# Performance work log

Measured on AMD Instinct MI355X. Metric: run time of the kernel, lower is better.

The kernel has to match this reference:

```python
import jax, jax.numpy as jnp
import numpy as np

B, N, C = 4, 1024, 1024
H = 16
HD = C // H
HID = 4 * C
EPS = 1e-5


def layernorm(x, g, b):
    mu = jnp.mean(x, axis=-1, keepdims=True)
    var = jnp.mean(jnp.square(x - mu), axis=-1, keepdims=True)
    return (x - mu) * jax.lax.rsqrt(var + EPS) * g + b


def setup_inputs() -> dict:
    key = jax.random.key(0)
    ks = jax.random.split(key, 16)
    s = lambda d: 1.0 / np.sqrt(d)
    return {
        "x": jax.random.normal(ks[0], (B, N, C), dtype=jnp.float32),
        "ln1_g": jnp.ones((C,), jnp.float32),
        "ln1_b": jnp.zeros((C,), jnp.float32),
        "qkv_w": jax.random.normal(ks[1], (3 * C, C), jnp.float32) * s(C),
        "proj_w": jax.random.normal(ks[2], (C, C), jnp.float32) * s(C),
        "proj_b": jnp.zeros((C,), jnp.float32),
        "gamma1": jnp.full((C,), 1e-5, jnp.float32),
        "ln2_g": jnp.ones((C,), jnp.float32),
        "ln2_b": jnp.zeros((C,), jnp.float32),
        "fc1_w": jax.random.normal(ks[3], (HID, C), jnp.float32) * s(C),
        "fc1_b": jnp.zeros((HID,), jnp.float32),
        "fc2_w": jax.random.normal(ks[4], (C, HID), jnp.float32) * s(HID),
        "fc2_b": jnp.zeros((C,), jnp.float32),
        "gamma2": jnp.full((C,), 1e-5, jnp.float32),
    }


def reference(x, ln1_g, ln1_b, qkv_w, proj_w, proj_b, gamma1,
              ln2_g, ln2_b, fc1_w, fc1_b, fc2_w, fc2_b, gamma2):
    # --- attention residual branch ---
    n1 = layernorm(x, ln1_g, ln1_b)                     # [B,N,C]
    qkv = jnp.einsum('bnc,oc->bno', n1, qkv_w)          # [B,N,3C]
    qkv = qkv.reshape(B, N, 3, H, HD).transpose(2, 0, 3, 1, 4)  # [3,B,H,N,HD]
    scale = HD ** -0.5
    q, k, v = qkv[0] * scale, qkv[1], qkv[2]
    attn = jax.nn.softmax(jnp.einsum('bhnd,bhmd->bhnm', q, k), axis=-1)  # [B,H,N,N]
    ao = jnp.einsum('bhnm,bhmd->bhnd', attn, v)         # [B,H,N,HD]
    ao = ao.transpose(0, 2, 1, 3).reshape(B, N, C)
    ao = jnp.einsum('bnc,oc->bno', ao, proj_w) + proj_b
    x = x + ao * gamma1
    # --- mlp residual branch ---
    n2 = layernorm(x, ln2_g, ln2_b)
    h = jax.nn.gelu(jnp.einsum('bnc,hc->bnh', n2, fc1_w) + fc1_b, approximate=False)
    m = jnp.einsum('bnh,ch->bnc', h, fc2_w) + fc2_b
    x = x + m * gamma2
    return x, attn
```

## Files before the change

kernel.cpp:

```cpp
#include <hip/hip_runtime.h>
#include <math.h>

typedef __attribute__((ext_vector_type(8))) short bf16x8;
typedef __attribute__((ext_vector_type(4))) short bf16x4;
typedef __attribute__((ext_vector_type(4))) float f32x4;

__device__ __forceinline__ unsigned short f2bf(float f) {
  unsigned u = __builtin_bit_cast(unsigned, f);
  u += 0x7fffu + ((u >> 16) & 1u);
  return (unsigned short)(u >> 16);
}

#define MFMA16(a, b, c) __builtin_amdgcn_mfma_f32_16x16x32_bf16((a), (b), (c), 0, 0, 0)

__device__ __forceinline__ void gload_lds16(const void* g, void* l) {
  __builtin_amdgcn_global_load_lds(
      (const __attribute__((address_space(1))) unsigned*)g,
      (__attribute__((address_space(3))) unsigned*)l, 16, 0, 0);
}

__device__ __forceinline__ int xcd_swz(int bid, int nwg) {
  int q = nwg >> 3, r = nwg & 7;
  int xcd = bid & 7, off = bid >> 3;
  return (xcd < r ? xcd * (q + 1) : r * (q + 1) + (xcd - r) * q) + off;
}

__global__ __launch_bounds__(256) void k_cvt4(
    const float* __restrict__ wq, const float* __restrict__ wp,
    const float* __restrict__ w1, const float* __restrict__ w2,
    unsigned short* __restrict__ oq, unsigned short* __restrict__ op,
    unsigned short* __restrict__ o1, unsigned short* __restrict__ o2) {
  int bid = blockIdx.x;
  const float* src; unsigned short* dst; int base;
  if (bid < 3072)      { src = wq; dst = oq; base = bid; }
  else if (bid < 4096) { src = wp; dst = op; base = bid - 3072; }
  else if (bid < 8192) { src = w1; dst = o1; base = bid - 4096; }
  else                 { src = w2; dst = o2; base = bid - 8192; }
  int i = base * 256 + threadIdx.x;
  float4 v = ((const float4*)src)[i];
  bf16x4 o;
  o[0] = (short)f2bf(v.x); o[1] = (short)f2bf(v.y);
  o[2] = (short)f2bf(v.z); o[3] = (short)f2bf(v.w);
  *(bf16x4*)(dst + (size_t)i * 4) = o;
}

__global__ __launch_bounds__(256) void k_ln(const float* __restrict__ x,
                                            const float* __restrict__ g,
                                            const float* __restrict__ b,
                                            unsigned short* __restrict__ out) {
  __shared__ float red[8];
  const int tid = threadIdx.x;
  const size_t row = blockIdx.x;
  float4 v = ((const float4*)(x + row * 1024))[tid];
  float s = v.x + v.y + v.z + v.w;
#pragma unroll
  for (int off = 32; off; off >>= 1) s += __shfl_xor(s, off);
  if ((tid & 63) == 0) red[tid >> 6] = s;
  __syncthreads();
  float mu = (red[0] + red[1] + red[2] + red[3]) * (1.0f / 1024.0f);
  float dx = v.x - mu, dy = v.y - mu, dz = v.z - mu, dw = v.w - mu;
  float s2 = dx * dx + dy * dy + dz * dz + dw * dw;
#pragma unroll
  for (int off = 32; off; off >>= 1) s2 += __shfl_xor(s2, off);
  if ((tid & 63) == 0) red[4 + (tid >> 6)] = s2;
  __syncthreads();
  float var = (red[4] + red[5] + red[6] + red[7]) * (1.0f / 1024.0f);
  float rstd = rsqrtf(var + 1e-5f);
  float4 gv = ((const float4*)g)[tid];
  float4 bv = ((const float4*)b)[tid];
  bf16x4 o;
  o[0] = (short)f2bf(dx * rstd * gv.x + bv.x);
  o[1] = (short)f2bf(dy * rstd * gv.y + bv.y);
  o[2] = (short)f2bf(dz * rstd * gv.z + bv.z);
  o[3] = (short)f2bf(dw * rstd * gv.w + bv.w);
  *(bf16x4*)(out + row * 1024 + tid * 4) = o;
}

template <int EPI>
__global__ __launch_bounds__(512, 2) void k_gemm256(
    const unsigned short* __restrict__ A, const unsigned short* __restrict__ Bw,
    int Ndim, int K, int nby,
    const float* __restrict__ bias,
    unsigned short* __restrict__ Qc, unsigned short* __restrict__ Kc,
    unsigned short* __restrict__ VTo,
    unsigned short* __restrict__ outb) {
  __shared__ __align__(16) unsigned short lds[2][2][16384];

  const int tid = threadIdx.x;
  const int wid = tid >> 6, lane = tid & 63;
  const int wm = wid >> 2, wn = wid & 3;
  const int lr = lane & 15, lhi = lane >> 4;

  const int nwg = gridDim.x;
  const int swz = xcd_swz(blockIdx.x, nwg);
  const int bcol = swz / nby, brow = swz % nby;

  const size_t a_base = (size_t)brow * 256 * K;
  const size_t b_base = (size_t)bcol * 256 * K;
  const int NT = K >> 6;

  auto STAGE = [&](int dbuf, int kt, int which) {
    int ktc = (kt < NT) ? kt : 0;
    int isB = which & 1;
    int odd = which >> 1;
    const unsigned short* src = isB ? (Bw + b_base) : (A + a_base);
    int col = (ktc << 6) + (((lane & 7) ^ ((lane >> 3) & 7)) << 3);
#pragma unroll
    for (int c = 0; c < 2; ++c) {
      int idx = (wid << 1) | c;
      int chunk = isB ? ((idx & 3) + ((idx >> 2) << 3) + (odd << 2))
                      : ((idx & 7) + ((idx >> 3) << 4) + (odd << 3));
      int row = (chunk << 3) + (lane >> 3);
      gload_lds16(src + (size_t)row * K + col,
                  &lds[dbuf][isB][chunk * 512 + lane * 8]);
    }
  };

  STAGE(0, 0, 0); STAGE(0, 0, 1); STAGE(0, 0, 2); STAGE(0, 0, 3);

  f32x4 acc[8][4] = {};
  bf16x8 aF0[4][2], aF1[4][2], bF0[2][2], bF1[2][2];

  const int colx0 = (lhi << 4) ^ ((lr & 7) << 4);
  const int colx1 = (64 + (lhi << 4)) ^ ((lr & 7) << 4);

  for (int t = 0; t < NT; ++t) {
    const int buf = t & 1;
    const char* sAb = (const char*)&lds[buf][0][0];
    const char* sBb = (const char*)&lds[buf][1][0];
#pragma unroll
    for (int q = 0; q < 4; ++q) {
      asm volatile("s_waitcnt vmcnt(6)" ::: "memory");
      __builtin_amdgcn_s_barrier();
      if (q == 0) {
#pragma unroll
        for (int m = 0; m < 4; ++m) {
          int ro = (wm * 128 + m * 16 + lr) * 128;
          aF0[m][0] = *(const bf16x8*)(sAb + ro + colx0);
          aF0[m][1] = *(const bf16x8*)(sAb + ro + colx1);
        }
      } else if (q == 1) {
#pragma unroll
        for (int n = 0; n < 2; ++n) {
          int ro = (wn * 64 + n * 16 + lr) * 128;
          bF0[n][0] = *(const bf16x8*)(sBb + ro + colx0);
          bF0[n][1] = *(const bf16x8*)(sBb + ro + colx1);
        }
      } else if (q == 2) {
#pragma unroll
        for (int m = 0; m < 4; ++m) {
          int ro = (wm * 128 + 64 + m * 16 + lr) * 128;
          aF1[m][0] = *(const bf16x8*)(sAb + ro + colx0);
          aF1[m][1] = *(const bf16x8*)(sAb + ro + colx1);
        }
      } else {
#pragma unroll
        for (int n = 0; n < 2; ++n) {
          int ro = (wn * 64 + 32 + n * 16 + lr) * 128;
          bF1[n][0] = *(const bf16x8*)(sBb + ro + colx0);
          bF1[n][1] = *(const bf16x8*)(sBb + ro + colx1);
        }
      }
      STAGE(buf ^ 1, t + 1, q);
      asm volatile("s_waitcnt lgkmcnt(0)" ::: "memory");
      __builtin_amdgcn_sched_barrier(0);
      __builtin_amdgcn_s_setprio(1);
      if (q == 0) {
        if (t > 0) {
#pragma unroll
          for (int m = 0; m < 4; ++m)
#pragma unroll
            for (int n = 0; n < 2; ++n)
#pragma unroll
              for (int kk = 0; kk < 2; ++kk)
                acc[4 + m][2 + n] = MFMA16(aF1[m][kk], bF1[n][kk], acc[4 + m][2 + n]);
        }
      } else if (q == 1) {
#pragma unroll
        for (int m = 0; m < 4; ++m)
#pragma unroll
          for (int n = 0; n < 2; ++n)
#pragma unroll
            for (int kk = 0; kk < 2; ++kk)
              acc[m][n] = MFMA16(aF0[m][kk], bF0[n][kk], acc[m][n]);
      } else if (q == 2) {
#pragma unroll
        for (int m = 0; m < 4; ++m)
#pragma unroll
          for (int n = 0; n < 2; ++n)
#pragma unroll
            for (int kk = 0; kk < 2; ++kk)
              acc[4 + m][n] = MFMA16(aF1[m][kk], bF0[n][kk], acc[4 + m][n]);
      } else {
#pragma unroll
        for (int m = 0; m < 4; ++m)
#pragma unroll
          for (int n = 0; n < 2; ++n)
#pragma unroll
            for (int kk = 0; kk < 2; ++kk)
              acc[m][2 + n] = MFMA16(aF0[m][kk], bF1[n][kk], acc[m][2 + n]);
      }
      __builtin_amdgcn_s_setprio(0);
    }
  }
#pragma unroll
  for (int m = 0; m < 4; ++m)
#pragma unroll
    for (int n = 0; n < 2; ++n)
#pragma unroll
      for (int kk = 0; kk < 2; ++kk)
        acc[4 + m][2 + n] = MFMA16(aF1[m][kk], bF1[n][kk], acc[4 + m][2 + n]);

  if (EPI == 0) {
    const int region = bcol >> 2;
    const int h = (bcol & 3) * 4 + wn;
    if (region < 2) {
      unsigned short* dst = (region == 0) ? Qc : Kc;
#pragma unroll
      for (int m = 0; m < 8; ++m)
#pragma unroll
        for (int n = 0; n < 4; ++n) {
          int d = n * 16 + lr;
#pragma unroll
          for (int r = 0; r < 4; ++r) {
            int row = brow * 256 + wm * 128 + m * 16 + lhi * 4 + r;
            int b = row >> 10, kv = row & 1023;
            dst[((size_t)((b << 4) + h) << 16) + (size_t)kv * 64 + d] =
                f2bf(acc[m][n][r]);
          }
        }
    } else {
#pragma unroll
      for (int m = 0; m < 8; ++m)
#pragma unroll
        for (int n = 0; n < 4; ++n) {
          int d = n * 16 + lr;
          int row0_ = brow * 256 + wm * 128 + m * 16 + lhi * 4;
          int b = row0_ >> 10, kv0 = row0_ & 1023;
          bf16x4 o;
          o[0] = (short)f2bf(acc[m][n][0]);
          o[1] = (short)f2bf(acc[m][n][1]);
          o[2] = (short)f2bf(acc[m][n][2]);
          o[3] = (short)f2bf(acc[m][n][3]);
          *(bf16x4*)&VTo[((size_t)((b << 4) + h) << 16) + ((size_t)d << 10) + kv0] = o;
        }
    }
  } else {
#pragma unroll
    for (int m = 0; m < 8; ++m)
#pragma unroll
      for (int n = 0; n < 4; ++n) {
        int col = bcol * 256 + wn * 64 + n * 16 + lr;
        float bi = bias[col];
#pragma unroll
        for (int r = 0; r < 4; ++r) {
          int row = brow * 256 + wm * 128 + m * 16 + lhi * 4 + r;
          float v = acc[m][n][r] + bi;
          v = 0.5f * v * (1.0f + erff(v * 0.70710678118654752f));
          outb[(size_t)row * Ndim + col] = f2bf(v);
        }
      }
  }
}

__global__ __launch_bounds__(256) void k_gemm_bt2(
    const unsigned short* __restrict__ A, const unsigned short* __restrict__ Bw,
    int Ndim, int K, int nby,
    const float* __restrict__ bias, const float* __restrict__ gamma,
    const float* __restrict__ resid, float* __restrict__ outf) {
  __shared__ __align__(16) unsigned short sA[128 * 64];
  __shared__ __align__(16) unsigned short sB[128 * 64];
  const int tid = threadIdx.x;
  const int wid = tid >> 6, lane = tid & 63;
  const int wr = wid >> 1, wc = wid & 1;
  const int lr = lane & 15, lhi = lane >> 4;
  const int swz = xcd_swz(blockIdx.x, gridDim.x);
  const int bcol = swz / nby, brow = swz % nby;

  const size_t a_base = (size_t)brow * 128 * K;
  const size_t b_base = (size_t)bcol * 128 * K;
  const int srow = tid >> 3;
  const int scol = (tid & 7) * 8;

  f32x4 acc[4][4] = {};

  for (int k0 = 0; k0 < K; k0 += 64) {
    __syncthreads();
#pragma unroll
    for (int r = 0; r < 4; ++r) {
      int row = r * 32 + srow;
      gload_lds16(&A[a_base + (size_t)row * K + k0 + scol], &sA[row * 64 + scol]);
      gload_lds16(&Bw[b_base + (size_t)row * K + k0 + scol], &sB[row * 64 + scol]);
    }
    __syncthreads();
#pragma unroll
    for (int kk = 0; kk < 2; ++kk) {
      bf16x8 af[4], bfr[4];
#pragma unroll
      for (int i = 0; i < 4; ++i) {
        int ar = wr * 64 + i * 16 + lr;
        af[i] = *(const bf16x8*)&sA[ar * 64 + kk * 32 + lhi * 8];
        int br = wc * 64 + i * 16 + lr;
        bfr[i] = *(const bf16x8*)&sB[br * 64 + kk * 32 + lhi * 8];
      }
#pragma unroll
      for (int i = 0; i < 4; ++i)
#pragma unroll
        for (int j = 0; j < 4; ++j)
          acc[i][j] = MFMA16(af[i], bfr[j], acc[i][j]);
    }
  }

#pragma unroll
  for (int i = 0; i < 4; ++i)
#pragma unroll
    for (int j = 0; j < 4; ++j)
#pragma unroll
      for (int r = 0; r < 4; ++r) {
        int row = brow * 128 + wr * 64 + i * 16 + lhi * 4 + r;
        int col = bcol * 128 + wc * 64 + j * 16 + lr;
        float v = resid[(size_t)row * Ndim + col] + (acc[i][j][r] + bias[col]) * gamma[col];
        outf[(size_t)row * Ndim + col] = v;
      }
}

__global__ __launch_bounds__(256) void k_attn(const unsigned short* __restrict__ Qc,
                                              const unsigned short* __restrict__ Kc,
                                              const unsigned short* __restrict__ VT,
                                              float* __restrict__ attn_out,
                                              unsigned short* __restrict__ ao) {
  __shared__ __align__(16) char smem[33280];
  __shared__ float red[2][4][32];

  const int tid = threadIdx.x;
  const int wid = tid >> 6, lane = tid & 63;
  const int lr = lane & 15, lhi = lane >> 4;
  const int q0 = blockIdx.x * 32;
  const int bh = blockIdx.y;
  const int b = bh >> 4, h = bh & 15;
  const size_t hb = (size_t)bh << 16;
  const int hcol = h * 64;

  bf16x8 af[2][2];
#pragma unroll
  for (int i = 0; i < 2; ++i)
#pragma unroll
    for (int kk = 0; kk < 2; ++kk)
      af[i][kk] = *(const bf16x8*)&Qc[hb + (size_t)(q0 + i * 16 + lr) * 64 +
                                      kk * 32 + lhi * 8];

  f32x4 acc[2][16] = {};
#pragma unroll
  for (int kk = 0; kk < 2; ++kk) {
#pragma unroll
    for (int j = 0; j < 16; ++j) {
      int m = wid * 256 + j * 16 + lr;
      bf16x8 bv = *(const bf16x8*)&Kc[hb + (size_t)m * 64 + kk * 32 + lhi * 8];
      acc[0][j] = MFMA16(af[0][kk], bv, acc[0][j]);
      acc[1][j] = MFMA16(af[1][kk], bv, acc[1][j]);
    }
  }

  float mx[2][4], sm[2][4];
#pragma unroll
  for (int i = 0; i < 2; ++i)
#pragma unroll
    for (int r = 0; r < 4; ++r) {
      float m_ = -1e30f;
#pragma unroll
      for (int j = 0; j < 16; ++j) {
        acc[i][j][r] *= 0.125f;
        m_ = fmaxf(m_, acc[i][j][r]);
      }
#pragma unroll
      for (int off = 1; off < 16; off <<= 1) m_ = fmaxf(m_, __shfl_xor(m_, off));
      mx[i][r] = m_;
    }
  if (lr == 0) {
#pragma unroll
    for (int i = 0; i < 2; ++i)
#pragma unroll
      for (int r = 0; r < 4; ++r) red[0][wid][i * 16 + lhi * 4 + r] = mx[i][r];
  }
  __syncthreads();
#pragma unroll
  for (int i = 0; i < 2; ++i)
#pragma unroll
    for (int r = 0; r < 4; ++r) {
      int rl = i * 16 + lhi * 4 + r;
      float m_ = fmaxf(fmaxf(red[0][0][rl], red[0][1][rl]),
                       fmaxf(red[0][2][rl], red[0][3][rl]));
      float s_ = 0.f;
#pragma unroll
      for (int j = 0; j < 16; ++j) {
        float e = __expf(acc[i][j][r] - m_);
        acc[i][j][r] = e;
        s_ += e;
      }
#pragma unroll
      for (int off = 1; off < 16; off <<= 1) s_ += __shfl_xor(s_, off);
      sm[i][r] = s_;
    }
  if (lr == 0) {
#pragma unroll
    for (int i = 0; i < 2; ++i)
#pragma unroll
      for (int r = 0; r < 4; ++r) red[1][wid][i * 16 + lhi * 4 + r] = sm[i][r];
  }
  __syncthreads();

  float inv[2][4];
#pragma unroll
  for (int i = 0; i < 2; ++i)
#pragma unroll
    for (int r = 0; r < 4; ++r) {
      int rl = i * 16 + lhi * 4 + r;
      inv[i][r] = 1.0f / (red[1][0][rl] + red[1][1][rl] + red[1][2][rl] + red[1][3][rl]);
    }

  unsigned pb[2][16][2];
  {
    const size_t attn_base =
        (size_t)bh * 1024 * 1024 + ((size_t)q0) * 1024 + (size_t)(wid * 256);
#pragma unroll
    for (int i = 0; i < 2; ++i)
#pragma unroll
      for (int j = 0; j < 16; ++j) {
        float p0 = acc[i][j][0] * inv[i][0];
        float p1 = acc[i][j][1] * inv[i][1];
        float p2 = acc[i][j][2] * inv[i][2];
        float p3 = acc[i][j][3] * inv[i][3];
        size_t base = attn_base + (size_t)(i * 16 + lhi * 4) * 1024 + j * 16 + lr;
        attn_out[base] = p0;
        attn_out[base + 1024] = p1;
        attn_out[base + 2048] = p2;
        attn_out[base + 3072] = p3;
        pb[i][j][0] = (unsigned)f2bf(p0) | ((unsigned)f2bf(p1) << 16);
        pb[i][j][1] = (unsigned)f2bf(p2) | ((unsigned)f2bf(p3) << 16);
      }
  }

  char* sP = smem + wid * 4096;
  f32x4 oaccT[4][2] = {};

#pragma unroll
  for (int t = 0; t < 4; ++t) {
#pragma unroll
    for (int i = 0; i < 2; ++i)
#pragma unroll
      for (int jl = 0; jl < 4; ++jl) {
        int j = t * 4 + jl;
        int kvl2 = (jl * 16 + lr) * 2;
#pragma unroll
        for (int hp = 0; hp < 2; ++hp) {
          unsigned d = pb[i][j][hp];
          int qa = i * 16 + lhi * 4 + hp * 2;
          int qb = qa + 1;
          *(unsigned short*)(sP + qa * 128 + (kvl2 ^ ((qa & 7) << 4))) =
              (unsigned short)(d & 0xffff);
          *(unsigned short*)(sP + qb * 128 + (kvl2 ^ ((qb & 7) << 4))) =
              (unsigned short)(d >> 16);
        }
      }
#pragma unroll
    for (int c = 0; c < 2; ++c) {
      bf16x8 pf[2];
#pragma unroll
      for (int qt = 0; qt < 2; ++qt) {
        int q_ = qt * 16 + lr;
        pf[qt] = *(const bf16x8*)(sP + q_ * 128 + ((c * 64 + lhi * 16) ^ ((q_ & 7) << 4)));
      }
#pragma unroll
      for (int dt = 0; dt < 4; ++dt) {
        int d_ = dt * 16 + lr;
        bf16x8 vf = *(const bf16x8*)&VT[hb + ((size_t)d_ << 10) +
                                        wid * 256 + t * 64 + c * 32 + lhi * 8];
        oaccT[dt][0] = MFMA16(vf, pf[0], oaccT[dt][0]);
        oaccT[dt][1] = MFMA16(vf, pf[1], oaccT[dt][1]);
      }
    }
  }

  __syncthreads();
  float* sAO = (float*)smem;
#pragma unroll
  for (int dt = 0; dt < 4; ++dt)
#pragma unroll
    for (int qt = 0; qt < 2; ++qt)
#pragma unroll
      for (int r = 0; r < 4; ++r) {
        int q_ = qt * 16 + lr;
        int d_ = dt * 16 + lhi * 4 + r;
        sAO[wid * 2080 + q_ * 65 + d_] = oaccT[dt][qt][r];
      }
  __syncthreads();
  {
    int q_ = tid >> 3;
    int d0 = (tid & 7) * 8;
    bf16x8 o;
#pragma unroll
    for (int e = 0; e < 8; ++e) {
      int d_ = d0 + e;
      float s = sAO[q_ * 65 + d_] + sAO[2080 + q_ * 65 + d_] +
                sAO[4160 + q_ * 65 + d_] + sAO[6240 + q_ * 65 + d_];
      o[e] = (short)f2bf(s);
    }
    *(bf16x8*)&ao[(size_t)(b * 1024 + q0 + q_) * 1024 + hcol + d0] = o;
  }
}

extern "C" void kernel_launch(void* const* d_in, const int* in_sizes, int n_in,
                              void* d_out, int out_size, void* d_ws, size_t ws_size,
                              hipStream_t stream) {
  (void)in_sizes; (void)n_in; (void)out_size; (void)ws_size;
  const float* x     = (const float*)d_in[0];
  const float* ln1g  = (const float*)d_in[1];
  const float* ln1b  = (const float*)d_in[2];
  const float* qkvw  = (const float*)d_in[3];
  const float* projw = (const float*)d_in[4];
  const float* projb = (const float*)d_in[5];
  const float* g1    = (const float*)d_in[6];
  const float* ln2g  = (const float*)d_in[7];
  const float* ln2b  = (const float*)d_in[8];
  const float* fc1w  = (const float*)d_in[9];
  const float* fc1b  = (const float*)d_in[10];
  const float* fc2w  = (const float*)d_in[11];
  const float* fc2b  = (const float*)d_in[12];
  const float* g2    = (const float*)d_in[13];

  char* ws = (char*)d_ws;
  unsigned short* w_qkv  = (unsigned short*)(ws);
  unsigned short* w_proj = (unsigned short*)(ws + 6291456);
  unsigned short* w_fc1  = (unsigned short*)(ws + 8388608);
  unsigned short* w_fc2  = (unsigned short*)(ws + 16777216);
  unsigned short* n12    = (unsigned short*)(ws + 25165824);
  unsigned short* Qc     = (unsigned short*)(ws + 33554432);
  unsigned short* Kc     = (unsigned short*)(ws + 41943040);
  unsigned short* VT     = (unsigned short*)(ws + 50331648);
  unsigned short* hbuf   = (unsigned short*)(ws + 33554432);
  unsigned short* aob    = (unsigned short*)(ws + 58720256);
  float*          x1     = (float*)(ws + 67108864);

  float* outx = (float*)d_out;
  float* outattn = outx + (size_t)4096 * 1024;

  k_cvt4<<<12288, 256, 0, stream>>>(qkvw, projw, fc1w, fc2w,
                                    w_qkv, w_proj, w_fc1, w_fc2);

  k_ln<<<4096, 256, 0, stream>>>(x, ln1g, ln1b, n12);
  k_gemm256<0><<<192, 512, 0, stream>>>(n12, w_qkv, 3072, 1024, 16,
                                        nullptr, Qc, Kc, VT, nullptr);
  k_attn<<<dim3(32, 64), 256, 0, stream>>>(Qc, Kc, VT, outattn, aob);
  k_gemm_bt2<<<256, 256, 0, stream>>>(aob, w_proj, 1024, 1024, 32,
                                      projb, g1, x, x1);
  k_ln<<<4096, 256, 0, stream>>>(x1, ln2g, ln2b, n12);
  k_gemm256<1><<<256, 512, 0, stream>>>(n12, w_fc1, 4096, 1024, 16,
                                        fc1b, nullptr, nullptr, nullptr, hbuf);
  k_gemm_bt2<<<256, 256, 0, stream>>>(hbuf, w_fc2, 1024, 4096, 32,
                                      fc2b, g2, x1, outx);
}
```

Baseline: 379.7 us.

## Split-K the fc2 GEMM with a reduction kernel and coalesce attention-prob stores

The fc2 GEMM (K=4096) now runs as a 4-way split-K over 1024 blocks instead of 256. Each slice writes fp32 partials to workspace, and a new reduction kernel sums them and applies bias, gamma and the residual. This raises parallelism on a GPU with many CUs, at the cost of extra partial-sum traffic (about 64MB written and read back). Separately, the attention kernel now writes the probability matrix from the swizzled LDS tile as row-contiguous float4 stores instead of scattered scalar stores. Those stored values are bf16-rounded probabilities rather than exact fp32, which costs some precision.

```diff
diff --git a/kernel.cpp b/kernel.cpp
--- a/kernel.cpp
+++ b/kernel.cpp
@@ -9,6 +9,9 @@
   unsigned u = __builtin_bit_cast(unsigned, f);
   u += 0x7fffu + ((u >> 16) & 1u);
   return (unsigned short)(u >> 16);
+}
+__device__ __forceinline__ float bf2f(unsigned short h) {
+  return __builtin_bit_cast(float, (unsigned)h << 16);
 }
 
 #define MFMA16(a, b, c) __builtin_amdgcn_mfma_f32_16x16x32_bf16((a), (b), (c), 0, 0, 0)
@@ -263,28 +266,34 @@
   }
 }
 
+template <int EPI>
 __global__ __launch_bounds__(256) void k_gemm_bt2(
     const unsigned short* __restrict__ A, const unsigned short* __restrict__ Bw,
     int Ndim, int K, int nby,
     const float* __restrict__ bias, const float* __restrict__ gamma,
-    const float* __restrict__ resid, float* __restrict__ outf) {
+    const float* __restrict__ resid, float* __restrict__ outf,
+    float* __restrict__ fpart) {
   __shared__ __align__(16) unsigned short sA[128 * 64];
   __shared__ __align__(16) unsigned short sB[128 * 64];
   const int tid = threadIdx.x;
   const int wid = tid >> 6, lane = tid & 63;
   const int wr = wid >> 1, wc = wid & 1;
   const int lr = lane & 15, lhi = lane >> 4;
-  const int swz = xcd_swz(blockIdx.x, gridDim.x);
+  int swz = xcd_swz(blockIdx.x, gridDim.x);
+  int kslice = 0;
+  if (EPI == 3) { kslice = swz & 3; swz >>= 2; }
   const int bcol = swz / nby, brow = swz % nby;
 
   const size_t a_base = (size_t)brow * 128 * K;
   const size_t b_base = (size_t)bcol * 128 * K;
   const int srow = tid >> 3;
   const int scol = (tid & 7) * 8;
+  const int kbeg = (EPI == 3) ? kslice * (K >> 2) : 0;
+  const int kend = (EPI == 3) ? kbeg + (K >> 2) : K;
 
   f32x4 acc[4][4] = {};
 
-  for (int k0 = 0; k0 < K; k0 += 64) {
+  for (int k0 = kbeg; k0 < kend; k0 += 64) {
     __syncthreads();
 #pragma unroll
     for (int r = 0; r < 4; ++r) {
@@ -311,6 +320,7 @@
     }
   }
 
+  const size_t pbase = (EPI == 3) ? (size_t)kslice * ((size_t)nby * 128) * Ndim : 0;
 #pragma unroll
   for (int i = 0; i < 4; ++i)
 #pragma unroll
@@ -319,9 +329,38 @@
       for (int r = 0; r < 4; ++r) {
         int row = brow * 128 + wr * 64 + i * 16 + lhi * 4 + r;
         int col = bcol * 128 + wc * 64 + j * 16 + lr;
-        float v = resid[(size_t)row * Ndim + col] + (acc[i][j][r] + bias[col]) * gamma[col];
-        outf[(size_t)row * Ndim + col] = v;
-      }
+        if (EPI == 2) {
+          float v = resid[(size_t)row * Ndim + col] +
+                    (acc[i][j][r] + bias[col]) * gamma[col];
+          outf[(size_t)row * Ndim + col] = v;
+        } else {
+          fpart[pbase + (size_t)row * Ndim + col] = acc[i][j][r];
+        }
+      }
+}
+
+__global__ __launch_bounds__(256) void k_fc2red(const float* __restrict__ p,
+                                                const float* __restrict__ x1,
+                                                const float* __restrict__ bias,
+                                                const float* __restrict__ gamma,
+                                                float* __restrict__ out) {
+  int idx = blockIdx.x * 256 + threadIdx.x;
+  int i = idx * 4;
+  int col = i & 1023;
+  const size_t S = (size_t)4096 * 1024;
+  float4 a = *(const float4*)&p[i];
+  float4 b = *(const float4*)&p[S + i];
+  float4 c = *(const float4*)&p[2 * S + i];
+  float4 d = *(const float4*)&p[3 * S + i];
+  float4 xr = *(const float4*)&x1[i];
+  float4 bi = *(const float4*)&bias[col];
+  float4 gm = *(const float4*)&gamma[col];
+  float4 o;
+  o.x = xr.x + (a.x + b.x + c.x + d.x + bi.x) * gm.x;
+  o.y = xr.y + (a.y + b.y + c.y + d.y + bi.y) * gm.y;
+  o.z = xr.z + (a.z + b.z + c.z + d.z + bi.z) * gm.z;
+  o.w = xr.w + (a.w + b.w + c.w + d.w + bi.w) * gm.w;
+  *(float4*)&out[i] = o;
 }
 
 __global__ __launch_bounds__(256) void k_attn(const unsigned short* __restrict__ Qc,
@@ -419,26 +458,15 @@
     }
 
   unsigned pb[2][16][2];
-  {
-    const size_t attn_base =
-        (size_t)bh * 1024 * 1024 + ((size_t)q0) * 1024 + (size_t)(wid * 256);
-#pragma unroll
-    for (int i = 0; i < 2; ++i)
-#pragma unroll
-      for (int j = 0; j < 16; ++j) {
-        float p0 = acc[i][j][0] * inv[i][0];
-        float p1 = acc[i][j][1] * inv[i][1];
-        float p2 = acc[i][j][2] * inv[i][2];
-        float p3 = acc[i][j][3] * inv[i][3];
-        size_t base = attn_base + (size_t)(i * 16 + lhi * 4) * 1024 + j * 16 + lr;
-        attn_out[base] = p0;
-        attn_out[base + 1024] = p1;
-        attn_out[base + 2048] = p2;
-        attn_out[base + 3072] = p3;
-        pb[i][j][0] = (unsigned)f2bf(p0) | ((unsigned)f2bf(p1) << 16);
-        pb[i][j][1] = (unsigned)f2bf(p2) | ((unsigned)f2bf(p3) << 16);
-      }
-  }
+#pragma unroll
+  for (int i = 0; i < 2; ++i)
+#pragma unroll
+    for (int j = 0; j < 16; ++j) {
+      pb[i][j][0] = (unsigned)f2bf(acc[i][j][0] * inv[i][0]) |
+                    ((unsigned)f2bf(acc[i][j][1] * inv[i][1]) << 16);
+      pb[i][j][1] = (unsigned)f2bf(acc[i][j][2] * inv[i][2]) |
+                    ((unsigned)f2bf(acc[i][j][3] * inv[i][3]) << 16);
+    }
 
   char* sP = smem + wid * 4096;
   f32x4 oaccT[4][2] = {};
@@ -462,6 +490,23 @@
               (unsigned short)(d >> 16);
         }
       }
+    {
+      int q_ = lane >> 1, half = lane & 1;
+      float* abase = attn_out + (size_t)bh * 1048576 + (size_t)(q0 + q_) * 1024 +
+                     wid * 256 + t * 64 + half * 32;
+#pragma unroll
+      for (int s = 0; s < 4; ++s) {
+        bf16x8 pv = *(const bf16x8*)(sP + q_ * 128 +
+                                     (((half * 32 + s * 8) * 2) ^ ((q_ & 7) << 4)));
+        float4 o0, o1;
+        o0.x = bf2f((unsigned short)pv[0]); o0.y = bf2f((unsigned short)pv[1]);
+        o0.z = bf2f((unsigned short)pv[2]); o0.w = bf2f((unsigned short)pv[3]);
+        o1.x = bf2f((unsigned short)pv[4]); o1.y = bf2f((unsigned short)pv[5]);
+        o1.z = bf2f((unsigned short)pv[6]); o1.w = bf2f((unsigned short)pv[7]);
+        *(float4*)(abase + s * 8) = o0;
+        *(float4*)(abase + s * 8 + 4) = o1;
+      }
+    }
 #pragma unroll
     for (int c = 0; c < 2; ++c) {
       bf16x8 pf[2];
@@ -540,6 +585,7 @@
   unsigned short* hbuf   = (unsigned short*)(ws + 33554432);
   unsigned short* aob    = (unsigned short*)(ws + 58720256);
   float*          x1     = (float*)(ws + 67108864);
+  float*          fpart  = (float*)(ws + 100663296);
 
   float* outx = (float*)d_out;
   float* outattn = outx + (size_t)4096 * 1024;
@@ -551,11 +597,12 @@
   k_gemm256<0><<<192, 512, 0, stream>>>(n12, w_qkv, 3072, 1024, 16,
                                         nullptr, Qc, Kc, VT, nullptr);
   k_attn<<<dim3(32, 64), 256, 0, stream>>>(Qc, Kc, VT, outattn, aob);
-  k_gemm_bt2<<<256, 256, 0, stream>>>(aob, w_proj, 1024, 1024, 32,
-                                      projb, g1, x, x1);
+  k_gemm_bt2<2><<<256, 256, 0, stream>>>(aob, w_proj, 1024, 1024, 32,
+                                         projb, g1, x, x1, nullptr);
   k_ln<<<4096, 256, 0, stream>>>(x1, ln2g, ln2b, n12);
   k_gemm256<1><<<256, 512, 0, stream>>>(n12, w_fc1, 4096, 1024, 16,
                                         fc1b, nullptr, nullptr, nullptr, hbuf);
-  k_gemm_bt2<<<256, 256, 0, stream>>>(hbuf, w_fc2, 1024, 4096, 32,
-                                      fc2b, g2, x1, outx);
-}
+  k_gemm_bt2<3><<<1024, 256, 0, stream>>>(hbuf, w_fc2, 1024, 4096, 32,
+                                          nullptr, nullptr, nullptr, nullptr, fpart);
+  k_fc2red<<<4096, 256, 0, stream>>>(fpart, x1, fc2b, g2, outx);
+}
```

New measurement: 438.0 us. +15.4%, slower.
